# Optimization experiments

Measured on AMD Instinct MI355X. Metric: run time of the kernel, lower is better.

The kernel has to match this reference:

```python
import jax, jax.numpy as jnp
import numpy as np

N, C_A, C_S, C_Z, H = 1024, 768, 384, 128, 16
D = C_A // H  # 48


def _ln(x, gamma=None, beta=None, eps=1e-5):
    m = jnp.mean(x, axis=-1, keepdims=True)
    v = jnp.var(x, axis=-1, keepdims=True)
    y = (x - m) * jax.lax.rsqrt(v + eps)
    if gamma is not None:
        y = y * gamma
    if beta is not None:
        y = y + beta
    return y


def _adaln(a, s, gamma_s, Wg, bg, Wadd):
    # AF3 Algorithm 26: LN(a) w/o affine, LN(s) w/ scale only; gate + additive shift from s
    a_ln = _ln(a)
    s_ln = _ln(s, gamma_s)
    return jax.nn.sigmoid(s_ln @ Wg + bg) * a_ln + s_ln @ Wadd


def setup_inputs() -> dict:
    key = jax.random.key(0)
    ks = iter(jax.random.split(key, 40))
    def nrm(shape, scale=0.02):
        return jax.random.normal(next(ks), shape, dtype=jnp.float32) * scale
    f32 = jnp.float32
    return dict(
        a=jax.random.normal(next(ks), (1, N, C_A), dtype=f32),
        s=jax.random.normal(next(ks), (1, N, C_S), dtype=f32),
        z=jax.random.normal(next(ks), (1, N, N, C_Z), dtype=f32),
        # AdaptiveLayerNorm (attention branch)
        gamma_s1=jnp.ones((C_S,), f32), Wg1=nrm((C_S, C_A)), bg1=jnp.zeros((C_A,), f32), Wadd1=nrm((C_S, C_A)),
        # pair-bias: LN(z) scale-only + LinearNoBias(c_z -> n_heads)
        gamma_z=jnp.ones((C_Z,), f32), Wz=nrm((C_Z, H)),
        # Attention: q has bias, k/v no bias, sigmoid gating, output proj
        Wq=nrm((C_A, C_A)), bq=jnp.zeros((C_A,), f32),
        Wk=nrm((C_A, C_A)), Wv=nrm((C_A, C_A)),
        Wgate=nrm((C_A, C_A)), bgate=jnp.ones((C_A,), f32),
        Wo=nrm((C_A, C_A)), bo=jnp.zeros((C_A,), f32),
        # BiasInitLinear output gate (biasinit=-2)
        Ws_last=nrm((C_S, C_A)), bs_last=jnp.full((C_A,), -2.0, f32),
        # ConditionedTransitionBlock (n=2)
        gamma_s2=jnp.ones((C_S,), f32), Wg2=nrm((C_S, C_A)), bg2=jnp.zeros((C_A,), f32), Wadd2=nrm((C_S, C_A)),
        W1=nrm((C_A, 2 * C_A)), W2=nrm((C_A, 2 * C_A)), Wb=nrm((2 * C_A, C_A)),
        Ws_t=nrm((C_S, C_A)), b_t=jnp.full((C_A,), -2.0, f32),
    )


def reference(a, s, z, gamma_s1, Wg1, bg1, Wadd1, gamma_z, Wz,
              Wq, bq, Wk, Wv, Wgate, bgate, Wo, bo, Ws_last, bs_last,
              gamma_s2, Wg2, bg2, Wadd2, W1, W2, Wb, Ws_t, b_t):
    B = a.shape[0]
    # ---- AttentionPairBias (standard / global path) ----
    a_ln = _adaln(a, s, gamma_s1, Wg1, bg1, Wadd1)
    bias = _ln(z, gamma_z) @ Wz                     # [B, N, N, H]
    bias = jnp.moveaxis(bias, -1, -3)               # [B, H, N, N]
    q = (a_ln @ Wq + bq).reshape(B, N, H, D)
    k = (a_ln @ Wk).reshape(B, N, H, D)
    v = (a_ln @ Wv).reshape(B, N, H, D)
    scale = 1.0 / float(np.sqrt(D))
    scores = jnp.einsum('bqhd,bkhd->bhqk', q, k) * scale + bias
    attn = jax.nn.softmax(scores, axis=-1)
    o = jnp.einsum('bhqk,bkhd->bqhd', attn, v)      # [B, N, H, D]
    g = jax.nn.sigmoid(a_ln @ Wgate + bgate).reshape(B, N, H, D)
    o = (g * o).reshape(B, N, C_A) @ Wo + bo
    attn_out = jax.nn.sigmoid(s @ Ws_last + bs_last) * o
    # ---- ConditionedTransitionBlock (Algorithm 25, n=2) ----
    a2 = _adaln(a, s, gamma_s2, Wg2, bg2, Wadd2)
    bmid = jax.nn.silu(a2 @ W1) * (a2 @ W2)
    t_out = jax.nn.sigmoid(s @ Ws_t + b_t) * (bmid @ Wb)
    # Algorithm 23 line 2-3: a = b + ConditionedTransitionBlock(a, s)
    return attn_out + t_out
```

## Files before the change

### kernel.cpp

```cpp
#include <hip/hip_runtime.h>

typedef __bf16 bf16;
typedef __bf16 v8bf __attribute__((ext_vector_type(8)));
typedef float  v4f  __attribute__((ext_vector_type(4)));
typedef short  short4v __attribute__((ext_vector_type(4)));

__device__ __forceinline__ float sigf(float x){ return 1.0f/(1.0f + __expf(-x)); }

typedef __attribute__((address_space(3))) unsigned int lds_u32;
typedef __attribute__((address_space(1))) const unsigned int gbl_u32;
__device__ __forceinline__ void gl16(const void* g, void* l) {
  __builtin_amdgcn_global_load_lds((gbl_u32*)g, (lds_u32*)l, 16, 0, 0);
}

struct WTab {
  const float* src[14];
  bf16* dst[14];
  int K[14], N[14], boff[14];
};

__device__ __forceinline__ void prepw_body(int bid, char* smem, const WTab& tab) {
  float (*lds)[33] = (float(*)[33])smem;
  int e = 0;
  #pragma unroll
  for (int i = 1; i < 14; i++) if (tab.boff[i] <= bid) e = i;
  int local = bid - tab.boff[e];
  int K = tab.K[e], N = tab.N[e];
  int nKT = K >> 5;
  int kt = local % nKT, nt = local / nKT;
  int k0 = kt * 32, n0 = nt * 32;
  const float* src = tab.src[e];
  bf16* dst = tab.dst[e];
  int tx = threadIdx.x & 31, ty = threadIdx.x >> 5;
  #pragma unroll
  for (int i = 0; i < 4; i++)
    lds[ty + i*8][tx] = src[(long)(k0 + ty + i*8) * N + n0 + tx];
  __syncthreads();
  #pragma unroll
  for (int i = 0; i < 4; i++)
    dst[(long)(n0 + ty + i*8) * K + k0 + tx] = (bf16)lds[tx][ty + i*8];
}

__device__ __forceinline__ void ln_a_body(int row, const float* __restrict__ a,
                                          float* __restrict__ out) {
  const float* x = a + (long)row * 768;
  int t = threadIdx.x;
  float lv[3], s = 0.f, q = 0.f;
  #pragma unroll
  for (int i = 0; i < 3; i++){ lv[i] = x[t + i*256]; s += lv[i]; q += lv[i]*lv[i]; }
  #pragma unroll
  for (int m = 1; m < 64; m <<= 1){ s += __shfl_xor(s, m); q += __shfl_xor(q, m); }
  __shared__ float ls[4], lq[4];
  int w = t >> 6, lane = t & 63;
  if (!lane){ ls[w] = s; lq[w] = q; }
  __syncthreads();
  s = ls[0]+ls[1]+ls[2]+ls[3]; q = lq[0]+lq[1]+lq[2]+lq[3];
  float mean = s * (1.f/768.f);
  float var  = q * (1.f/768.f) - mean*mean;
  float inv  = rsqrtf(var + 1e-5f);
  float* o = out + (long)row * 768;
  #pragma unroll
  for (int i = 0; i < 3; i++) o[t + i*256] = (lv[i] - mean) * inv;
}

__device__ __forceinline__ void ln_s_body(int row, const float* __restrict__ sIn,
    const float* __restrict__ g1, const float* __restrict__ g2,
    bf16* __restrict__ s1, bf16* __restrict__ s2, bf16* __restrict__ sb) {
  int t = threadIdx.x & 127;
  int sub = threadIdx.x >> 7;
  int r = row*2 + sub;
  const float* x = sIn + (long)r * 384;
  float lv[3], s = 0.f, q = 0.f;
  #pragma unroll
  for (int i = 0; i < 3; i++){ lv[i] = x[t + i*128]; s += lv[i]; q += lv[i]*lv[i]; }
  #pragma unroll
  for (int m = 1; m < 64; m <<= 1){ s += __shfl_xor(s, m); q += __shfl_xor(q, m); }
  __shared__ float ls[2][2], lq[2][2];
  int w = (t >> 6) & 1, lane = t & 63;
  if (!lane){ ls[sub][w] = s; lq[sub][w] = q; }
  __syncthreads();
  s = ls[sub][0] + ls[sub][1]; q = lq[sub][0] + lq[sub][1];
  float mean = s * (1.f/384.f);
  float var  = q * (1.f/384.f) - mean*mean;
  float inv  = rsqrtf(var + 1e-5f);
  long base = (long)r * 384;
  #pragma unroll
  for (int i = 0; i < 3; i++){
    int c = t + i*128;
    float y = (lv[i] - mean) * inv;
    s1[base + c] = (bf16)(y * g1[c]);
    s2[base + c] = (bf16)(y * g2[c]);
    sb[base + c] = (bf16)lv[i];
  }
}

__global__ __launch_bounds__(256) void k_prep(WTab tab, int boffTot,
    const float* Wz, const float* gz, bf16* wzT,
    const float* A_in, float* alnr,
    const float* S_in, const float* g1, const float* g2,
    bf16* sl1, bf16* sl2, bf16* sbf)
{
  __shared__ __align__(16) char smem[4224];
  int bid = blockIdx.x;
  if (bid < boffTot) { prepw_body(bid, smem, tab); return; }
  bid -= boffTot;
  if (bid < 8) {
    int t = bid * 256 + threadIdx.x;
    int k = t >> 4, h = t & 15;
    wzT[h * 128 + k] = (bf16)(Wz[t] * gz[k]);
    return;
  }
  bid -= 8;
  if (bid < 1024) { ln_a_body(bid, A_in, alnr); return; }
  bid -= 1024;
  ln_s_body(bid, S_in, g1, g2, sl1, sl2, sbf);
}

__device__ __forceinline__ void zbias_body(int bid, char* smem,
    const float* __restrict__ z, const bf16* __restrict__ wzT,
    bf16* __restrict__ biasb) {
  float (*pb)[17] = (float(*)[17])smem;
  int t = threadIdx.x, lane = t & 63, w = t >> 6;
  int r16 = lane & 15, g4 = lane >> 4;
  long base = (long)bid * 64;
  long pos = base + w*16 + r16;
  const float* zr = z + pos * 128;
  float4 xv[8];
  #pragma unroll
  for (int s = 0; s < 4; s++) {
    xv[2*s]   = *reinterpret_cast<const float4*>(&zr[s*32 + g4*8]);
    xv[2*s+1] = *reinterpret_cast<const float4*>(&zr[s*32 + g4*8 + 4]);
  }
  const float* x = reinterpret_cast<const float*>(xv);
  float sm = 0.f, q = 0.f;
  #pragma unroll
  for (int i = 0; i < 32; i++){ sm += x[i]; q += x[i]*x[i]; }
  sm += __shfl_xor(sm, 16); q += __shfl_xor(q, 16);
  sm += __shfl_xor(sm, 32); q += __shfl_xor(q, 32);
  float mean = sm * (1.f/128.f), var = q * (1.f/128.f) - mean*mean;
  float inv = rsqrtf(var + 1e-5f);
  v4f acc = (v4f){0.f, 0.f, 0.f, 0.f};
  #pragma unroll
  for (int s = 0; s < 4; s++) {
    union { bf16 b[8]; v8bf v; } ua;
    #pragma unroll
    for (int j = 0; j < 8; j++) ua.b[j] = (bf16)((x[s*8 + j] - mean) * inv);
    v8bf bw = *reinterpret_cast<const v8bf*>(&wzT[r16*128 + s*32 + g4*8]);
    acc = __builtin_amdgcn_mfma_f32_16x16x32_bf16(ua.v, bw, acc, 0, 0, 0);
  }
  #pragma unroll
  for (int r = 0; r < 4; r++) pb[w*16 + g4*4 + r][r16] = acc[r];
  __syncthreads();
  int p = t & 63, hb = t >> 6;
  #pragma unroll
  for (int j = 0; j < 4; j++) {
    int h = hb*4 + j;
    biasb[((long)h << 20) + base + p] = (bf16)pb[p][h];
  }
}

#define EPI_ADASG  0
#define EPI_SWIGLU 1
#define EPI_QKVG   2
#define EPI_WO     6
#define EPI_WB     7

template<int TM, int TN, bool DUAL, int EPI>
__device__ __forceinline__ void gemm_body(
    bf16* As, bf16* Bs, int m0, int n0, int z,
    const bf16* __restrict__ Ap, const bf16* __restrict__ B1, long sBpair, int K,
    const float* __restrict__ f0, const float* __restrict__ f1,
    const float* __restrict__ f2, const float* __restrict__ f3,
    const float* __restrict__ f4, const bf16* __restrict__ bb0,
    void* __restrict__ outp, long sOutz)
{
  constexpr int WM = TM/2, WN = TN/2;
  constexpr int MI = WM/16, NI = WN/16;
  const bf16* B2 = B1 + sBpair;
  int t = threadIdx.x, lane = t & 63, w = t >> 6;
  int wr = w >> 1, wc = w & 1;
  int r16 = lane & 15, g4 = lane >> 4;
  constexpr int NACC = DUAL ? 2 : 1;
  v4f acc[NACC][MI][NI];
  #pragma unroll
  for (int d = 0; d < NACC; d++)
    #pragma unroll
    for (int mi = 0; mi < MI; mi++)
      #pragma unroll
      for (int ni = 0; ni < NI; ni++)
        acc[d][mi][ni] = (v4f){0.f, 0.f, 0.f, 0.f};

  for (int k0 = 0; k0 < K; k0 += 64) {
    #pragma unroll
    for (int cb = 0; cb < TM/32; cb++) {
      int cc = cb*4 + w;
      int c16 = cc*64 + lane;
      int row = c16 >> 3, col = c16 & 7;
      int scol = col ^ (row & 7);
      gl16(&Ap[(long)(m0 + row)*K + k0 + scol*8], (char*)As + cc*1024);
    }
    #pragma unroll
    for (int cb = 0; cb < TN/32; cb++) {
      int cc = cb*4 + w;
      int c16 = cc*64 + lane;
      int row = c16 >> 3, col = c16 & 7;
      int scol = col ^ (row & 7);
      gl16(&B1[(long)(n0 + row)*K + k0 + scol*8], (char*)Bs + cc*1024);
      if constexpr (DUAL)
        gl16(&B2[(long)(n0 + row)*K + k0 + scol*8], (char*)Bs + TN*128 + cc*1024);
    }
    __syncthreads();
    #pragma unroll
    for (int s = 0; s < 2; s++) {
      int ch = s*4 + g4;
      v8bf af[MI];
      #pragma unroll
      for (int mi = 0; mi < MI; mi++) {
        int ra = wr*WM + mi*16 + r16;
        af[mi] = *reinterpret_cast<const v8bf*>(
            (const char*)As + ra*128 + ((ch ^ (ra & 7)) << 4));
      }
      #pragma unroll
      for (int d = 0; d < NACC; d++)
        #pragma unroll
        for (int ni = 0; ni < NI; ni++) {
          int rb = wc*WN + ni*16 + r16;
          v8bf bfv = *reinterpret_cast<const v8bf*>(
              (const char*)Bs + d*(TN*128) + rb*128 + ((ch ^ (rb & 7)) << 4));
          #pragma unroll
          for (int mi = 0; mi < MI; mi++)
            acc[d][mi][ni] = __builtin_amdgcn_mfma_f32_16x16x32_bf16(af[mi], bfv, acc[d][mi][ni], 0, 0, 0);
        }
    }
    __syncthreads();
  }

  int colb = n0 + wc*WN + r16;
  int rowb = m0 + wr*WM + (g4 << 2);
  #pragma unroll
  for (int mi = 0; mi < MI; mi++)
    #pragma unroll
    for (int ni = 0; ni < NI; ni++) {
      int col = colb + ni*16;
      if constexpr (EPI == EPI_ADASG) {
        if (z < 2) {
          float bg = (z == 0 ? f1 : f2)[col];
          bf16* o = (bf16*)outp + (long)z * sOutz;
          #pragma unroll
          for (int r = 0; r < 4; r++) {
            long idx = (long)(rowb + mi*16 + r)*768 + col;
            float gl = acc[0][mi][ni][r] + bg;
            o[idx] = (bf16)(sigf(gl) * f0[idx] + acc[1][mi][ni][r]);
          }
        } else {
          bf16* o0 = (bf16*)outp + 2*sOutz;
          bf16* o1 = (bf16*)outp + 3*sOutz;
          #pragma unroll
          for (int r = 0; r < 4; r++) {
            long idx = (long)(rowb + mi*16 + r)*768 + col;
            o0[idx] = (bf16)sigf(acc[0][mi][ni][r] + f3[col]);
            o1[idx] = (bf16)sigf(acc[1][mi][ni][r] + f4[col]);
          }
        }
      } else if constexpr (EPI == EPI_SWIGLU) {
        bf16* o = (bf16*)outp;
        #pragma unroll
        for (int r = 0; r < 4; r++) {
          long idx = (long)(rowb + mi*16 + r)*1536 + col;
          float x1 = acc[0][mi][ni][r], x2 = acc[1][mi][ni][r];
          o[idx] = (bf16)(x1 * sigf(x1) * x2);
        }
      } else if constexpr (EPI == EPI_QKVG) {
        int h = col / 48, d = col - h*48;
        if (z == 0) {
          const float qs = 0.14433756729740643f;
          bf16* qp = (bf16*)outp;
          #pragma unroll
          for (int r = 0; r < 4; r++)
            qp[(long)h*65536 + (long)(rowb + mi*16 + r)*64 + d] =
              (bf16)((acc[0][mi][ni][r] + f0[col]) * qs);
        } else if (z == 1) {
          bf16* kp = (bf16*)outp + sOutz;
          #pragma unroll
          for (int r = 0; r < 4; r++)
            kp[(long)h*65536 + (long)(rowb + mi*16 + r)*64 + d] = (bf16)acc[0][mi][ni][r];
        } else if (z == 2) {
          bf16* vT = (bf16*)outp + 2*sOutz;
          union { bf16 h4[4]; short4v s4; } u;
          #pragma unroll
          for (int r = 0; r < 4; r++) u.h4[r] = (bf16)acc[0][mi][ni][r];
          *reinterpret_cast<short4v*>(&vT[(long)h*65536 + (long)d*1024 + rowb + mi*16]) = u.s4;
        } else {
          bf16* gp = (bf16*)outp + 3*sOutz;
          #pragma unroll
          for (int r = 0; r < 4; r++)
            gp[(long)(rowb + mi*16 + r)*768 + col] = (bf16)sigf(acc[0][mi][ni][r] + f1[col]);
        }
      } else if constexpr (EPI == EPI_WO) {
        float* o = (float*)outp;
        #pragma unroll
        for (int r = 0; r < 4; r++) {
          long idx = (long)(rowb + mi*16 + r)*768 + col;
          o[idx] = o[idx] + (float)bb0[idx] * (acc[0][mi][ni][r] + f0[col]);
        }
      } else {
        float* o = (float*)outp;
        #pragma unroll
        for (int r = 0; r < 4; r++) {
          long idx = (long)(rowb + mi*16 + r)*768 + col;
          o[idx] = (float)bb0[idx] * acc[0][mi][ni][r];
        }
      }
    }
}

template<int TM, int TN, bool DUAL, int EPI>
__global__ __launch_bounds__(256) void gemm_k(
    const bf16* A, const bf16* B, long sAz, long sBz, long sBpair, int K,
    const float* f0, const float* f1, const float* f2, const float* f3,
    const float* f4, const bf16* bb0, void* outp, long sOutz)
{
  __shared__ __align__(16) bf16 As[TM*64];
  __shared__ __align__(16) bf16 Bs[(DUAL?2:1)*TN*64];
  int z = blockIdx.z;
  gemm_body<TM,TN,DUAL,EPI>(As, Bs, blockIdx.y*TM, blockIdx.x*TN, z,
      A + (long)z*sAz, B + (long)z*sBz, sBpair, K,
      f0, f1, f2, f3, f4, bb0, outp, sOutz);
}

__global__ __launch_bounds__(256, 4) void k_mega(
    const bf16* aln, const bf16* wQKVG, const float* bq, const float* bgate,
    bf16* qkv, const bf16* a2b, const bf16* wW12, bf16* bmid,
    const float* Zin, const bf16* wzT, bf16* biasb)
{
  __shared__ __align__(16) char smem[24576];
  int bid = blockIdx.x;
  if (bid < 768) {
    int z = bid / 192, rem = bid % 192;
    gemm_body<64,64,false,EPI_QKVG>((bf16*)smem, (bf16*)(smem + 8192),
        (rem/12)*64, (rem%12)*64, z,
        aln, wQKVG + (long)z*589824, 0, 768,
        bq, bgate, nullptr, nullptr, nullptr, nullptr, qkv, 1048576);
  } else if (bid < 1152) {
    int rem = bid - 768;
    gemm_body<64,64,true,EPI_SWIGLU>((bf16*)smem, (bf16*)(smem + 8192),
        (rem/24)*64, (rem%24)*64, 0,
        a2b, wW12, 1179648, 768,
        nullptr, nullptr, nullptr, nullptr, nullptr, nullptr, bmid, 0);
  } else {
    zbias_body(bid - 1152, smem, Zin, wzT, biasb);
  }
}

__device__ __forceinline__ void flash_body(int qt, int h, char* smem,
    const bf16* __restrict__ qp, const bf16* __restrict__ kp,
    const bf16* __restrict__ vT, const bf16* __restrict__ biasb,
    const bf16* __restrict__ gp, bf16* __restrict__ gob)
{
  int t = threadIdx.x, lane = t & 63, w = t >> 6;
  int q0 = qt * 64 + w * 16;
  int r16 = lane & 15, g4 = lane >> 4;
  bf16* plw = (bf16*)smem + w * 1152;
  const bf16* qb = qp + ((long)h << 16);
  const bf16* kb = kp + ((long)h << 16);
  const bf16* vb = vT + ((long)h << 16);
  const bf16* bb = biasb + ((long)h << 20) + (long)q0 * 1024;

  v8bf qa[2];
  #pragma unroll
  for (int s = 0; s < 2; s++)
    qa[s] = *reinterpret_cast<const v8bf*>(&qb[(long)(q0 + r16)*64 + s*32 + g4*8]);

  v4f oacc[4];
  #pragma unroll
  for (int nd = 0; nd < 4; nd++) oacc[nd] = (v4f){0.f, 0.f, 0.f, 0.f};
  float mrun[4], lrun[4];
  #pragma unroll
  for (int r = 0; r < 4; r++){ mrun[r] = -1e30f; lrun[r] = 0.f; }

  for (int kt = 0; kt < 16; kt++) {
    int k0 = kt * 64;
    v4f sacc[4];
    #pragma unroll
    for (int nk = 0; nk < 4; nk++) sacc[nk] = (v4f){0.f, 0.f, 0.f, 0.f};
    #pragma unroll
    for (int nk = 0; nk < 4; nk++)
      #pragma unroll
      for (int s = 0; s < 2; s++) {
        v8bf kf = *reinterpret_cast<const v8bf*>(&kb[(long)(k0 + nk*16 + r16)*64 + s*32 + g4*8]);
        sacc[nk] = __builtin_amdgcn_mfma_f32_16x16x32_bf16(qa[s], kf, sacc[nk], 0, 0, 0);
      }
    float mtile[4];
    #pragma unroll
    for (int r = 0; r < 4; r++) mtile[r] = -1e30f;
    #pragma unroll
    for (int nk = 0; nk < 4; nk++)
      #pragma unroll
      for (int r = 0; r < 4; r++) {
        float bvv = (float)bb[(long)(g4*4 + r)*1024 + k0 + nk*16 + r16];
        sacc[nk][r] += bvv;
        mtile[r] = fmaxf(mtile[r], sacc[nk][r]);
      }
    #pragma unroll
    for (int r = 0; r < 4; r++) {
      #pragma unroll
      for (int m = 1; m < 16; m <<= 1) mtile[r] = fmaxf(mtile[r], __shfl_xor(mtile[r], m));
    }
    float scl[4], rsum[4];
    #pragma unroll
    for (int r = 0; r < 4; r++) {
      float mn = fmaxf(mrun[r], mtile[r]);
      scl[r] = __expf(mrun[r] - mn);
      mrun[r] = mn;
      rsum[r] = 0.f;
    }
    #pragma unroll
    for (int nk = 0; nk < 4; nk++)
      #pragma unroll
      for (int r = 0; r < 4; r++) {
        float p = __expf(sacc[nk][r] - mrun[r]);
        rsum[r] += p;
        plw[(g4*4 + r)*72 + nk*16 + r16] = (bf16)p;
      }
    #pragma unroll
    for (int r = 0; r < 4; r++) {
      #pragma unroll
      for (int m = 1; m < 16; m <<= 1) rsum[r] += __shfl_xor(rsum[r], m);
      lrun[r] = lrun[r]*scl[r] + rsum[r];
      #pragma unroll
      for (int nd = 0; nd < 4; nd++) oacc[nd][r] *= scl[r];
    }
    v8bf pa[2];
    #pragma unroll
    for (int s = 0; s < 2; s++)
      pa[s] = *reinterpret_cast<const v8bf*>(&plw[r16*72 + s*32 + g4*8]);
    #pragma unroll
    for (int nd = 0; nd < 4; nd++)
      #pragma unroll
      for (int s = 0; s < 2; s++) {
        v8bf vf = *reinterpret_cast<const v8bf*>(&vb[(long)(nd*16 + r16)*1024 + k0 + s*32 + g4*8]);
        oacc[nd] = __builtin_amdgcn_mfma_f32_16x16x32_bf16(pa[s], vf, oacc[nd], 0, 0, 0);
      }
  }
  #pragma unroll
  for (int r = 0; r < 4; r++) {
    int qrow = q0 + g4*4 + r;
    float invl = 1.0f / lrun[r];
    #pragma unroll
    for (int nd = 0; nd < 3; nd++) {
      long idx = (long)qrow*768 + h*48 + nd*16 + r16;
      gob[idx] = (bf16)(oacc[nd][r] * invl * (float)gp[idx]);
    }
  }
}

__global__ __launch_bounds__(256) void k_tail(
    const bf16* bmid, const bf16* wWbT, const bf16* sgf1, float* OUT,
    const bf16* qp, const bf16* kp, const bf16* vT, const bf16* biasb,
    const bf16* gp, bf16* gob)
{
  __shared__ __align__(16) char smem[16384];
  int bid = blockIdx.x;
  if (bid < 192) {
    gemm_body<64,64,false,EPI_WB>((bf16*)smem, (bf16*)(smem + 8192),
        (bid/12)*64, (bid%12)*64, 0,
        bmid, wWbT, 0, 1536,
        nullptr, nullptr, nullptr, nullptr, nullptr, sgf1, OUT, 0);
  } else {
    int local = bid - 192;
    flash_body(local & 15, local >> 4, smem, qp, kp, vT, biasb, gp, gob);
  }
}

extern "C" void kernel_launch(void* const* d_in, const int* in_sizes, int n_in,
                              void* d_out, int out_size, void* d_ws, size_t ws_size,
                              hipStream_t stream)
{
  const float* A_in  = (const float*)d_in[0];
  const float* S_in  = (const float*)d_in[1];
  const float* Z_in  = (const float*)d_in[2];
  const float* g_s1  = (const float*)d_in[3];
  const float* Wg1   = (const float*)d_in[4];
  const float* bg1   = (const float*)d_in[5];
  const float* Wadd1 = (const float*)d_in[6];
  const float* g_z   = (const float*)d_in[7];
  const float* Wz    = (const float*)d_in[8];
  const float* Wq    = (const float*)d_in[9];
  const float* bq    = (const float*)d_in[10];
  const float* Wk    = (const float*)d_in[11];
  const float* Wv    = (const float*)d_in[12];
  const float* Wgate = (const float*)d_in[13];
  const float* bgate = (const float*)d_in[14];
  const float* Wo    = (const float*)d_in[15];
  const float* bo    = (const float*)d_in[16];
  const float* WsL   = (const float*)d_in[17];
  const float* bsL   = (const float*)d_in[18];
  const float* g_s2  = (const float*)d_in[19];
  const float* Wg2   = (const float*)d_in[20];
  const float* bg2   = (const float*)d_in[21];
  const float* Wadd2 = (const float*)d_in[22];
  const float* W1    = (const float*)d_in[23];
  const float* W2    = (const float*)d_in[24];
  const float* Wb    = (const float*)d_in[25];
  const float* WsT   = (const float*)d_in[26];
  const float* b_t   = (const float*)d_in[27];
  float* OUT = (float*)d_out;

  char* ws = (char*)d_ws;
  size_t off = 0;
  auto alloc = [&](size_t bytes) -> void* {
    void* p = ws + off; off += (bytes + 255) & ~(size_t)255; return p; };

  bf16*  wGA6  = (bf16*) alloc(6ul*294912*2);
  bf16*  wQKVG = (bf16*) alloc(4ul*589824*2);
  bf16*  wWoT  = (bf16*) alloc(589824ul*2);
  bf16*  wW12  = (bf16*) alloc(2ul*1179648*2);
  bf16*  wWbT  = (bf16*) alloc(1179648ul*2);
  bf16*  wzT   = (bf16*) alloc(2048ul*2);
  bf16*  sl1   = (bf16*) alloc(393216ul*2);
  bf16*  sl2   = (bf16*) alloc(393216ul*2);
  bf16*  sbf   = (bf16*) alloc(393216ul*2);
  float* alnr  = (float*)alloc(786432ul*4);
  bf16*  aln   = (bf16*) alloc(786432ul*2);
  bf16*  a2b   = (bf16*) alloc(786432ul*2);
  bf16*  sgf   = (bf16*) alloc(2ul*786432*2);
  bf16*  qkv   = (bf16*) alloc((3ul*1048576 + 786432)*2);
  bf16*  biasb = (bf16*) alloc(16777216ul*2);
  bf16*  gob   = (bf16*) alloc(786432ul*2);
  bf16*  bmid  = (bf16*) alloc(1572864ul*2);

  WTab tab;
  auto setw = [&](int i, const float* src, bf16* dst, int K, int N){
    tab.src[i] = src; tab.dst[i] = dst; tab.K[i] = K; tab.N[i] = N; };
  setw(0,  Wg1,   wGA6,             384,  768);
  setw(1,  Wadd1, wGA6 + 294912,    384,  768);
  setw(2,  Wg2,   wGA6 + 589824,    384,  768);
  setw(3,  Wadd2, wGA6 + 884736,    384,  768);
  setw(4,  WsL,   wGA6 + 1179648,   384,  768);
  setw(5,  WsT,   wGA6 + 1474560,   384,  768);
  setw(6,  Wq,    wQKVG,            768,  768);
  setw(7,  Wk,    wQKVG + 589824,   768,  768);
  setw(8,  Wv,    wQKVG + 2*589824, 768,  768);
  setw(9,  Wgate, wQKVG + 3*589824, 768,  768);
  setw(10, Wo,    wWoT,             768,  768);
  setw(11, W1,    wW12,             768, 1536);
  setw(12, W2,    wW12 + 1179648,   768, 1536);
  setw(13, Wb,    wWbT,            1536,  768);
  int boff = 0;
  for (int i = 0; i < 14; i++){ tab.boff[i] = boff; boff += (tab.K[i]/32)*(tab.N[i]/32); }

  (void)hipMemsetAsync(qkv, 0, 3ul*1048576*2, stream);

  k_prep<<<boff + 8 + 1024 + 512, 256, 0, stream>>>(
      tab, boff, Wz, g_z, wzT, A_in, alnr, S_in, g_s1, g_s2, sl1, sl2, sbf);

  gemm_k<64,64,true,EPI_ADASG><<<dim3(12,16,3), 256, 0, stream>>>(
      sl1, wGA6, 393216, 589824, 294912, 384,
      alnr, bg1, bg2, bsL, b_t, nullptr, aln, 786432);

  k_mega<<<17536, 256, 0, stream>>>(
      aln, wQKVG, bq, bgate, qkv, a2b, wW12, bmid, Z_in, wzT, biasb);

  k_tail<<<448, 256, 0, stream>>>(
      bmid, wWbT, sgf + 786432, OUT,
      qkv, qkv + 1048576, qkv + 2097152, biasb, qkv + 3145728, gob);

  gemm_k<64,64,false,EPI_WO><<<dim3(12,16,1), 256, 0, stream>>>(
      gob, wWoT, 0, 0, 0, 768,
      bo, nullptr, nullptr, nullptr, nullptr, sgf, OUT, 0);
}
```

Before: 272.8 us.

## Rebalance kernel fusion: merge AdaLN GEMM with z-bias, split flash and Wb GEMM

The AdaLN/gate GEMM is fused into a new first mega-kernel together with part of the z pair-bias work (ZSPLIT blocks), and the rest of the z-bias goes into the second mega-kernel. The QKVG GEMM there now uses 128x128 tiles with larger shared memory and fewer blocks. Flash attention becomes its own kernel, and the Wb GEMM moves after the Wo GEMM, which writes to a temporary buffer that Wb then adds into OUT. The aim is to overlap the bandwidth-heavy z-bias pass with GEMMs and to cut per-block overhead, at the cost of an extra fp32 round trip and an extra launch.

```diff
diff --git a/kernel.cpp b/kernel.cpp
--- a/kernel.cpp
+++ b/kernel.cpp
@@ -63,12 +63,12 @@
   for (int i = 0; i < 3; i++) o[t + i*256] = (lv[i] - mean) * inv;
 }
 
-__device__ __forceinline__ void ln_s_body(int row, const float* __restrict__ sIn,
+__device__ __forceinline__ void ln_s_body(int rowpair, const float* __restrict__ sIn,
     const float* __restrict__ g1, const float* __restrict__ g2,
     bf16* __restrict__ s1, bf16* __restrict__ s2, bf16* __restrict__ sb) {
   int t = threadIdx.x & 127;
   int sub = threadIdx.x >> 7;
-  int r = row*2 + sub;
+  int r = rowpair*2 + sub;
   const float* x = sIn + (long)r * 384;
   float lv[3], s = 0.f, q = 0.f;
   #pragma unroll
@@ -301,14 +301,14 @@
         #pragma unroll
         for (int r = 0; r < 4; r++) {
           long idx = (long)(rowb + mi*16 + r)*768 + col;
-          o[idx] = o[idx] + (float)bb0[idx] * (acc[0][mi][ni][r] + f0[col]);
+          o[idx] = (float)bb0[idx] * (acc[0][mi][ni][r] + f0[col]);
         }
       } else {
         float* o = (float*)outp;
         #pragma unroll
         for (int r = 0; r < 4; r++) {
           long idx = (long)(rowb + mi*16 + r)*768 + col;
-          o[idx] = (float)bb0[idx] * acc[0][mi][ni][r];
+          o[idx] = f0[idx] + (float)bb0[idx] * acc[0][mi][ni][r];
         }
       }
     }
@@ -328,39 +328,60 @@
       f0, f1, f2, f3, f4, bb0, outp, sOutz);
 }
 
-__global__ __launch_bounds__(256, 4) void k_mega(
+#define ZSPLIT 5120
+
+__global__ __launch_bounds__(256, 4) void k_mega_a(
+    const bf16* sl1, const bf16* wGA6, const float* alnr,
+    const float* bg1, const float* bg2, const float* bsL, const float* b_t,
+    bf16* aln, const float* Zin, const bf16* wzT, bf16* biasb)
+{
+  __shared__ __align__(16) char smem[24576];
+  int bid = blockIdx.x;
+  if (bid < 576) {
+    int z = bid / 192, rem = bid % 192;
+    gemm_body<64,64,true,EPI_ADASG>((bf16*)smem, (bf16*)(smem + 8192),
+        (rem/12)*64, (rem%12)*64, z,
+        sl1 + (long)z*393216, wGA6 + (long)z*589824, 294912, 384,
+        alnr, bg1, bg2, bsL, b_t, nullptr, aln, 786432);
+  } else {
+    zbias_body(bid - 576, smem, Zin, wzT, biasb);
+  }
+}
+
+__global__ __launch_bounds__(256, 3) void k_mega_b(
     const bf16* aln, const bf16* wQKVG, const float* bq, const float* bgate,
     bf16* qkv, const bf16* a2b, const bf16* wW12, bf16* bmid,
     const float* Zin, const bf16* wzT, bf16* biasb)
 {
-  __shared__ __align__(16) char smem[24576];
+  __shared__ __align__(16) char smem[32768];
   int bid = blockIdx.x;
-  if (bid < 768) {
-    int z = bid / 192, rem = bid % 192;
-    gemm_body<64,64,false,EPI_QKVG>((bf16*)smem, (bf16*)(smem + 8192),
-        (rem/12)*64, (rem%12)*64, z,
+  if (bid < 192) {
+    int z = bid / 48, rem = bid % 48;
+    gemm_body<128,128,false,EPI_QKVG>((bf16*)smem, (bf16*)(smem + 16384),
+        (rem/6)*128, (rem%6)*128, z,
         aln, wQKVG + (long)z*589824, 0, 768,
         bq, bgate, nullptr, nullptr, nullptr, nullptr, qkv, 1048576);
-  } else if (bid < 1152) {
-    int rem = bid - 768;
+  } else if (bid < 576) {
+    int rem = bid - 192;
     gemm_body<64,64,true,EPI_SWIGLU>((bf16*)smem, (bf16*)(smem + 8192),
         (rem/24)*64, (rem%24)*64, 0,
         a2b, wW12, 1179648, 768,
         nullptr, nullptr, nullptr, nullptr, nullptr, nullptr, bmid, 0);
   } else {
-    zbias_body(bid - 1152, smem, Zin, wzT, biasb);
-  }
-}
-
-__device__ __forceinline__ void flash_body(int qt, int h, char* smem,
+    zbias_body(bid - 576 + ZSPLIT, smem, Zin, wzT, biasb);
+  }
+}
+
+__global__ __launch_bounds__(256) void k_flash(
     const bf16* __restrict__ qp, const bf16* __restrict__ kp,
     const bf16* __restrict__ vT, const bf16* __restrict__ biasb,
     const bf16* __restrict__ gp, bf16* __restrict__ gob)
 {
+  __shared__ bf16 pl[4][16*72];
   int t = threadIdx.x, lane = t & 63, w = t >> 6;
-  int q0 = qt * 64 + w * 16;
+  int h = blockIdx.y;
+  int q0 = blockIdx.x * 64 + w * 16;
   int r16 = lane & 15, g4 = lane >> 4;
-  bf16* plw = (bf16*)smem + w * 1152;
   const bf16* qb = qp + ((long)h << 16);
   const bf16* kb = kp + ((long)h << 16);
   const bf16* vb = vT + ((long)h << 16);
@@ -414,6 +435,7 @@
       mrun[r] = mn;
       rsum[r] = 0.f;
     }
+    bf16* plw = &pl[w][0];
     #pragma unroll
     for (int nk = 0; nk < 4; nk++)
       #pragma unroll
@@ -451,24 +473,6 @@
       long idx = (long)qrow*768 + h*48 + nd*16 + r16;
       gob[idx] = (bf16)(oacc[nd][r] * invl * (float)gp[idx]);
     }
-  }
-}
-
-__global__ __launch_bounds__(256) void k_tail(
-    const bf16* bmid, const bf16* wWbT, const bf16* sgf1, float* OUT,
-    const bf16* qp, const bf16* kp, const bf16* vT, const bf16* biasb,
-    const bf16* gp, bf16* gob)
-{
-  __shared__ __align__(16) char smem[16384];
-  int bid = blockIdx.x;
-  if (bid < 192) {
-    gemm_body<64,64,false,EPI_WB>((bf16*)smem, (bf16*)(smem + 8192),
-        (bid/12)*64, (bid%12)*64, 0,
-        bmid, wWbT, 0, 1536,
-        nullptr, nullptr, nullptr, nullptr, nullptr, sgf1, OUT, 0);
-  } else {
-    int local = bid - 192;
-    flash_body(local & 15, local >> 4, smem, qp, kp, vT, biasb, gp, gob);
   }
 }
 
@@ -527,6 +531,7 @@
   bf16*  qkv   = (bf16*) alloc((3ul*1048576 + 786432)*2);
   bf16*  biasb = (bf16*) alloc(16777216ul*2);
   bf16*  gob   = (bf16*) alloc(786432ul*2);
+  float* opj   = (float*)alloc(786432ul*4);
   bf16*  bmid  = (bf16*) alloc(1572864ul*2);
 
   WTab tab;
@@ -554,18 +559,20 @@
   k_prep<<<boff + 8 + 1024 + 512, 256, 0, stream>>>(
       tab, boff, Wz, g_z, wzT, A_in, alnr, S_in, g_s1, g_s2, sl1, sl2, sbf);
 
-  gemm_k<64,64,true,EPI_ADASG><<<dim3(12,16,3), 256, 0, stream>>>(
-      sl1, wGA6, 393216, 589824, 294912, 384,
-      alnr, bg1, bg2, bsL, b_t, nullptr, aln, 786432);
-
-  k_mega<<<17536, 256, 0, stream>>>(
+  k_mega_a<<<576 + ZSPLIT, 256, 0, stream>>>(
+      sl1, wGA6, alnr, bg1, bg2, bsL, b_t, aln, Z_in, wzT, biasb);
+
+  k_mega_b<<<576 + (16384 - ZSPLIT), 256, 0, stream>>>(
       aln, wQKVG, bq, bgate, qkv, a2b, wW12, bmid, Z_in, wzT, biasb);
 
-  k_tail<<<448, 256, 0, stream>>>(
-      bmid, wWbT, sgf + 786432, OUT,
+  k_flash<<<dim3(16,16), 256, 0, stream>>>(
       qkv, qkv + 1048576, qkv + 2097152, biasb, qkv + 3145728, gob);
 
   gemm_k<64,64,false,EPI_WO><<<dim3(12,16,1), 256, 0, stream>>>(
       gob, wWoT, 0, 0, 0, 768,
-      bo, nullptr, nullptr, nullptr, nullptr, sgf, OUT, 0);
-}
+      bo, nullptr, nullptr, nullptr, nullptr, sgf, opj, 0);
+
+  gemm_k<64,64,false,EPI_WB><<<dim3(12,16,1), 256, 0, stream>>>(
+      bmid, wWbT, 0, 0, 0, 1536,
+      opj, nullptr, nullptr, nullptr, nullptr, sgf + 786432, OUT, 0);
+}
```

Result: faster. 232.8 us, median of 2 (-14.7%).
